# Kernel optimization log

Hardware: AMD Instinct MI355X
Metric: run time of the kernel (lower is better)

Reference implementation:

```python
import jax, jax.numpy as jnp
import numpy as np

B, C, H, W, K = 2, 64, 192, 192, 7
PAD = K // 2
EPS = 1e-6


def _win_idx(L):
    # NATTEN border handling: window is shifted (not zero-padded) to stay in-bounds.
    i = jnp.arange(L)
    start = jnp.clip(i - PAD, 0, L - K)            # [L] window start per query pos
    win = start[:, None] + jnp.arange(K)[None]     # [L,K] absolute key positions
    pb = (K - 1) - (i - start)                     # [L] rpb start index per query pos
    pbi = pb[:, None] + jnp.arange(K)[None]        # [L,K] rpb table indices
    return win, pbi


def setup_inputs() -> dict:
    key = jax.random.key(0)
    ks = jax.random.split(key, 10)
    g = jax.random.normal(ks[0], (B, C, H, W), jnp.float32)
    cd = jax.random.uniform(ks[1], (B, 1, H, W), dtype=jnp.float32)
    dense = jax.random.uniform(ks[2], (B, 1, H, W), dtype=jnp.float32)
    sel = jax.random.uniform(ks[3], (B, 1, H, W)) < 0.05
    sd = jnp.where(sel, dense, 0.0)
    mask = (jax.random.uniform(ks[4], (B, 1, H, W)) < 0.5).astype(jnp.float32)
    ln_w = 1.0 + 0.02 * jax.random.normal(ks[5], (C,), jnp.float32)
    ln_b = 0.02 * jax.random.normal(ks[6], (C,), jnp.float32)
    conv_w = 0.05 * jax.random.normal(ks[7], (2 * C, C + 1), jnp.float32)  # 1x1 conv
    conv_b = 0.02 * jax.random.normal(ks[8], (2 * C,), jnp.float32)
    rpb = 0.02 * jax.random.normal(ks[9], (1, 2 * K - 1, 2 * K - 1), jnp.float32)
    return {"g": g, "cd": cd, "sd": sd, "mask": mask,
            "ln_w": ln_w, "ln_b": ln_b, "conv_w": conv_w, "conv_b": conv_b, "rpb": rpb}


def reference(g, cd, sd, mask, ln_w, ln_b, conv_w, conv_b, rpb):
    # LayerNorm2d: normalize over channel dim per spatial location
    mu = g.mean(axis=1, keepdims=True)
    var = ((g - mu) ** 2).mean(axis=1, keepdims=True)
    gn = (g - mu) * jax.lax.rsqrt(var + EPS)
    gn = gn * ln_w[None, :, None, None] + ln_b[None, :, None, None]

    z = jnp.concatenate([gn, cd], axis=1)                      # [B,C+1,H,W]
    qk = jnp.einsum('bchw,oc->bohw', z, conv_w) + conv_b[None, :, None, None]
    q, k = qk[:, :C], qk[:, C:]
    k = k * mask

    qc = q.transpose(0, 2, 3, 1)                               # [B,H,W,C] single head
    kc = k.transpose(0, 2, 3, 1)
    rwin, rpbi = _win_idx(H)
    cwin, cpbi = _win_idx(W)

    # NATTEN qk + relative position bias over 7x7 neighborhoods
    k_win = kc[:, rwin][:, :, :, cwin]                         # [B,H,K,W,K,C]
    attn = jnp.einsum('bhwc,bhiwjc->bhwij', qc, k_win)         # [B,H,W,K,K]
    bias = rpb[0][rpbi][:, :, cpbi]                            # [H,K,W,K]
    attn = attn + bias.transpose(0, 2, 1, 3)[None]
    a = jax.nn.softmax(attn.reshape(B, H, W, K * K), axis=-1).reshape(B, H, W, K, K)

    # NATTEN av with v = cd (head_dim 1)
    v_win = cd[:, 0][:, rwin][:, :, :, cwin]                   # [B,H,K,W,K]
    cd_out = jnp.einsum('bhwij,bhiwj->bhw', a, v_win)[:, None]  # [B,1,H,W]
    m_win = mask[:, 0][:, rwin][:, :, :, cwin]
    mask_out = jnp.einsum('bhwij,bhiwj->bhw', a, m_win)[:, None]

    # NYU / SDR post-processing
    cd_out = cd_out * mask + cd * (1.0 - mask)
    valid = sd > 0
    cd_out = jnp.where(valid, sd, cd_out)
    mask_out = jnp.where(valid, mask, mask_out)
    return cd_out, mask_out
```

## Files before the change

### kernel.cpp

```cpp
#include <hip/hip_runtime.h>

constexpr int NB = 2;
constexpr int NC = 64;
constexpr int NH = 192;
constexpr int NW = 192;
constexpr int NK = 7;
constexpr int NHW = NH * NW;
constexpr int NPIX = NB * NHW;
constexpr float EPS = 1e-6f;

__global__ __launch_bounds__(256) void qk_gemm(
    const float* __restrict__ g, const float* __restrict__ cd,
    const float* __restrict__ mask,
    const float* __restrict__ ln_w, const float* __restrict__ ln_b,
    const float* __restrict__ conv_w, const float* __restrict__ conv_b,
    float* __restrict__ qbuf, float* __restrict__ kbuf)
{
    __shared__ float Z[65][128];
    __shared__ float WTc[33][128];

    int tid = threadIdx.x;
    int p0 = blockIdx.x * 128;
    int b  = p0 / NHW;
    int hw0 = p0 - b * NHW;

    int px = tid >> 1;
    int hf = tid & 1;
    const float* gp = g + (size_t)(b * NC + hf * 32) * NHW + (hw0 + px);
    float vals[32];
    float s = 0.f, sq = 0.f;
#pragma unroll
    for (int j = 0; j < 32; ++j) {
        float v = gp[(size_t)j * NHW];
        vals[j] = v; s += v; sq += v * v;
    }
    s  += __shfl_xor(s, 1);
    sq += __shfl_xor(sq, 1);
    float mu   = s * (1.f / 64.f);
    float rstd = rsqrtf(sq * (1.f / 64.f) - mu * mu + EPS);
#pragma unroll
    for (int j = 0; j < 32; ++j) {
        int c = hf * 32 + j;
        Z[c][px] = (vals[j] - mu) * rstd * ln_w[c] + ln_b[c];
    }
    if (hf) Z[64][px] = cd[p0 + px];

    int og = tid >> 4;
    int pg = tid & 15;
    float acc[8][8];
#pragma unroll
    for (int oi = 0; oi < 8; ++oi)
#pragma unroll
        for (int pj = 0; pj < 8; ++pj) acc[oi][pj] = 0.f;

    for (int cc = 0; cc < 65; cc += 33) {
        int nr = (65 - cc < 33) ? (65 - cc) : 33;
        __syncthreads();
        if (tid < 128) {
            int o = tid;
            for (int r = 0; r < nr; ++r)
                WTc[r][o] = conv_w[o * 65 + cc + r];
        }
        __syncthreads();
        for (int r = 0; r < nr; ++r) {
            float4 w0 = *(const float4*)&WTc[r][8 * og];
            float4 w1 = *(const float4*)&WTc[r][8 * og + 4];
            float4 z0 = *(const float4*)&Z[cc + r][8 * pg];
            float4 z1 = *(const float4*)&Z[cc + r][8 * pg + 4];
            float w8[8] = {w0.x, w0.y, w0.z, w0.w, w1.x, w1.y, w1.z, w1.w};
            float z8[8] = {z0.x, z0.y, z0.z, z0.w, z1.x, z1.y, z1.z, z1.w};
#pragma unroll
            for (int oi = 0; oi < 8; ++oi)
#pragma unroll
                for (int pj = 0; pj < 8; ++pj)
                    acc[oi][pj] = fmaf(w8[oi], z8[pj], acc[oi][pj]);
        }
    }

    int o0  = og * 8;
    int pxb = pg * 8;
    float4 ba = *(const float4*)&conv_b[o0];
    float4 bb = *(const float4*)&conv_b[o0 + 4];
    float bia[8] = {ba.x, ba.y, ba.z, ba.w, bb.x, bb.y, bb.z, bb.w};
    bool isq = (o0 < 64);
    float m8[8];
    if (!isq) {
        float4 ma = *(const float4*)&mask[p0 + pxb];
        float4 mc = *(const float4*)&mask[p0 + pxb + 4];
        m8[0]=ma.x; m8[1]=ma.y; m8[2]=ma.z; m8[3]=ma.w;
        m8[4]=mc.x; m8[5]=mc.y; m8[6]=mc.z; m8[7]=mc.w;
    }
    float* base = isq ? (qbuf + (size_t)(b * NC + o0) * NHW + hw0 + pxb)
                      : (kbuf + (size_t)(b * NC + o0 - 64) * NHW + hw0 + pxb);
#pragma unroll
    for (int oi = 0; oi < 8; ++oi) {
        float v[8];
#pragma unroll
        for (int pj = 0; pj < 8; ++pj) {
            float t = acc[oi][pj] + bia[oi];
            v[pj] = isq ? t : t * m8[pj];
        }
        float* dst = base + (size_t)oi * NHW;
        *(float4*)&dst[0] = make_float4(v[0], v[1], v[2], v[3]);
        *(float4*)&dst[4] = make_float4(v[4], v[5], v[6], v[7]);
    }
}

__global__ __launch_bounds__(512) void attn_tile(
    const float* __restrict__ qbuf, const float* __restrict__ kbuf,
    const float* __restrict__ cd, const float* __restrict__ sd,
    const float* __restrict__ mask, const float* __restrict__ rpb,
    float* __restrict__ out_cd, float* __restrict__ out_mask)
{
    __shared__ float kst[8][2][240];
    __shared__ float cdt[14 * 24];
    __shared__ float mt [14 * 24];
    __shared__ float rpbt[169];
    __shared__ float xch[128][49];

    int tid  = threadIdx.x;
    int g    = tid >> 6;
    int lane = tid & 63;
    int rq   = g & 1;
    int quar = g >> 1;
    int tx   = lane & 15;
    int tyw  = lane >> 4;

    int bid = blockIdx.x;
    int swz = (bid & 7) * 72 + (bid >> 3);
    int bw = swz % 12;
    int t2 = swz / 12;
    int bh = t2 % 24;
    int b  = t2 / 24;
    int w0 = bw * 16, h0 = bh * 8;
    int hr0 = h0 + rq * 4;

    int h = hr0 + tyw;
    int w = w0 + tx;
    int rs = min(max(h - 3, 0), NH - NK);
    int cs = min(max(w - 3, 0), NW - NK);
    int rb  = (rs - (hr0 - 3)) * 24 + (cs - (w0 - 3));
    int rbB = (rs - (h0  - 3)) * 24 + (cs - (w0 - 3));

    const float* cdb = cd   + (size_t)b * NHW;
    const float* msb = mask + (size_t)b * NHW;
    for (int e = tid; e < 308; e += 512) {
        int r = e / 22, c2 = e - r * 22;
        int gr = min(max(h0 - 3 + r, 0), NH - 1);
        int gc = min(max(w0 - 3 + c2, 0), NW - 1);
        cdt[r * 24 + c2] = cdb[gr * NW + gc];
        mt [r * 24 + c2] = msb[gr * NW + gc];
    }
    if (tid < 169) rpbt[tid] = rpb[tid];

    int soff[4], slds[4]; bool sact[4];
#pragma unroll
    for (int s = 0; s < 4; ++s) {
        int e = lane + 64 * s;
        int r = e / 22, c2 = e - r * 22;
        int gr = min(max(hr0 - 3 + r, 0), NH - 1);
        int gc = min(max(w0 - 3 + c2, 0), NW - 1);
        soff[s] = gr * NW + gc;
        slds[s] = r * 24 + c2;
        sact[s] = (e < 220);
    }

    const float* kb = kbuf + (size_t)(b * NC + quar * 16) * NHW;
    const float* qb = qbuf + (size_t)(b * NC + quar * 16) * NHW + h * NW + w;

    float at[49];
#pragma unroll
    for (int n = 0; n < 49; ++n) at[n] = 0.f;

    float st[4];
#pragma unroll
    for (int s = 0; s < 4; ++s) st[s] = sact[s] ? kb[soff[s]] : 0.f;
    float* k0 = kst[g][0];
    float* k1 = kst[g][1];
#pragma unroll
    for (int s = 0; s < 4; ++s) if (sact[s]) k0[slds[s]] = st[s];
    float qA = qb[0];
    float qB = qb[NHW];

    for (int i = 0; i < 16; ++i) {
        if (i + 1 < 16) {
            const float* kb2 = kb + (size_t)(i + 1) * NHW;
#pragma unroll
            for (int s = 0; s < 4; ++s) st[s] = sact[s] ? kb2[soff[s]] : 0.f;
        }
        float q = qA;
        qA = qB;
        if (i + 2 < 16) qB = qb[(size_t)(i + 2) * NHW];
        const float* kt = ((i & 1) ? k1 : k0) + rb;
#pragma unroll
        for (int r = 0; r < 7; ++r)
#pragma unroll
            for (int j = 0; j < 7; ++j)
                at[r * 7 + j] = fmaf(q, kt[r * 24 + j], at[r * 7 + j]);
        if (i + 1 < 16) {
            float* nk = (i & 1) ? k0 : k1;
#pragma unroll
            for (int s = 0; s < 4; ++s) if (sact[s]) nk[slds[s]] = st[s];
        }
    }

    int pxid = (rq * 4 + tyw) * 16 + tx;
    if (quar == 3) {
#pragma unroll
        for (int n = 0; n < 49; ++n) xch[pxid][n] = at[n];
    }
    __syncthreads();
    if (quar == 2) {
#pragma unroll
        for (int n = 0; n < 49; ++n) xch[pxid][n] += at[n];
    }
    __syncthreads();
    if (quar == 1) {
#pragma unroll
        for (int n = 0; n < 49; ++n) xch[pxid][n] += at[n];
    }
    __syncthreads();
    int pr = 6 - (h - rs);
    int pc = 6 - (w - cs);
    if (quar == 0) {
#pragma unroll
        for (int n = 0; n < 49; ++n) at[n] += xch[pxid][n];
#pragma unroll
        for (int r = 0; r < 7; ++r)
#pragma unroll
            for (int j = 0; j < 7; ++j)
                at[r * 7 + j] += rpbt[(pr + r) * 13 + pc + j];
#pragma unroll
        for (int n = 0; n < 49; ++n) xch[pxid][n] = at[n];
    }
    __syncthreads();
    if (quar >= 2) return;
    if (quar == 1) {
#pragma unroll
        for (int n = 0; n < 49; ++n) at[n] = xch[pxid][n];
    }

    float mx = -1e30f;
#pragma unroll
    for (int n = 0; n < 49; ++n) mx = fmaxf(mx, at[n]);
    float sm = 0.f;
#pragma unroll
    for (int n = 0; n < 49; ++n) {
        at[n] = __expf(at[n] - mx);
        sm += at[n];
    }

    const float* vt = (quar ? mt : cdt) + rbB;
    float sv = 0.f;
#pragma unroll
    for (int r = 0; r < 7; ++r)
#pragma unroll
        for (int j = 0; j < 7; ++j)
            sv = fmaf(at[r * 7 + j], vt[r * 24 + j], sv);
    sv /= sm;

    int p = b * NHW + h * NW + w;
    float sdc = sd[p];
    int cidx = (rq * 4 + tyw + 3) * 24 + (tx + 3);
    float mc = mt[cidx];
    if (quar == 0) {
        float cdc = cdt[cidx];
        float co = sv * mc + cdc * (1.f - mc);
        if (sdc > 0.f) co = sdc;
        out_cd[p] = co;
    } else {
        out_mask[p] = (sdc > 0.f) ? mc : sv;
    }
}

extern "C" void kernel_launch(void* const* d_in, const int* in_sizes, int n_in,
                              void* d_out, int out_size, void* d_ws, size_t ws_size,
                              hipStream_t stream) {
    const float* g      = (const float*)d_in[0];
    const float* cd     = (const float*)d_in[1];
    const float* sd     = (const float*)d_in[2];
    const float* mask   = (const float*)d_in[3];
    const float* ln_w   = (const float*)d_in[4];
    const float* ln_b   = (const float*)d_in[5];
    const float* conv_w = (const float*)d_in[6];
    const float* conv_b = (const float*)d_in[7];
    const float* rpb    = (const float*)d_in[8];

    float* out  = (float*)d_out;
    float* qbuf = (float*)d_ws;
    float* kbuf = qbuf + (size_t)NB * NC * NHW;

    qk_gemm<<<dim3(NPIX / 128), dim3(256), 0, stream>>>(
        g, cd, mask, ln_w, ln_b, conv_w, conv_b, qbuf, kbuf);
    attn_tile<<<dim3(NB * 24 * 12), dim3(512), 0, stream>>>(
        qbuf, kbuf, cd, sd, mask, rpb, out, out + NPIX);
}
```

Before: 147.5 us.

## Compute two adjacent pixels per thread in attention tile to reuse key loads

```diff
diff --git a/kernel.cpp b/kernel.cpp
--- a/kernel.cpp
+++ b/kernel.cpp
@@ -106,25 +106,26 @@
     }
 }
 
-__global__ __launch_bounds__(512) void attn_tile(
+struct TrueC  { static constexpr bool value = true;  };
+struct FalseC { static constexpr bool value = false; };
+
+__global__ __launch_bounds__(256) void attn_tile(
     const float* __restrict__ qbuf, const float* __restrict__ kbuf,
     const float* __restrict__ cd, const float* __restrict__ sd,
     const float* __restrict__ mask, const float* __restrict__ rpb,
     float* __restrict__ out_cd, float* __restrict__ out_mask)
 {
-    __shared__ float kst[8][2][240];
-    __shared__ float cdt[14 * 24];
-    __shared__ float mt [14 * 24];
+    __shared__ float kst[4][2][350];
+    __shared__ float xch[49][2][64];
+    __shared__ float cdt[350];
+    __shared__ float mt [350];
     __shared__ float rpbt[169];
-    __shared__ float xch[128][49];
 
     int tid  = threadIdx.x;
     int g    = tid >> 6;
     int lane = tid & 63;
-    int rq   = g & 1;
-    int quar = g >> 1;
-    int tx   = lane & 15;
-    int tyw  = lane >> 4;
+    int tx   = lane & 7;
+    int ty   = lane >> 3;
 
     int bid = blockIdx.x;
     int swz = (bid & 7) * 72 + (bid >> 3);
@@ -133,143 +134,187 @@
     int bh = t2 % 24;
     int b  = t2 / 24;
     int w0 = bw * 16, h0 = bh * 8;
-    int hr0 = h0 + rq * 4;
-
-    int h = hr0 + tyw;
-    int w = w0 + tx;
-    int rs = min(max(h - 3, 0), NH - NK);
-    int cs = min(max(w - 3, 0), NW - NK);
-    int rb  = (rs - (hr0 - 3)) * 24 + (cs - (w0 - 3));
-    int rbB = (rs - (h0  - 3)) * 24 + (cs - (w0 - 3));
+
+    int h   = h0 + ty;
+    int wpx = w0 + 2 * tx;
+    int rs  = min(max(h - 3, 0), NH - NK);
+    int cs0 = min(max(wpx - 3, 0), NW - NK);
+    int cs1 = min(max(wpx - 2, 0), NW - NK);
+    int d1  = cs1 - cs0;
+    int ktb = (rs - (h0 - 3)) * 25 + (cs0 - (w0 - 3));
 
     const float* cdb = cd   + (size_t)b * NHW;
     const float* msb = mask + (size_t)b * NHW;
-    for (int e = tid; e < 308; e += 512) {
-        int r = e / 22, c2 = e - r * 22;
+    for (int e = tid; e < 308; e += 256) {
+        int r = e / 22, c = e - r * 22;
         int gr = min(max(h0 - 3 + r, 0), NH - 1);
-        int gc = min(max(w0 - 3 + c2, 0), NW - 1);
-        cdt[r * 24 + c2] = cdb[gr * NW + gc];
-        mt [r * 24 + c2] = msb[gr * NW + gc];
+        int gc = min(max(w0 - 3 + c, 0), NW - 1);
+        cdt[r * 25 + c] = cdb[gr * NW + gc];
+        mt [r * 25 + c] = msb[gr * NW + gc];
     }
     if (tid < 169) rpbt[tid] = rpb[tid];
 
-    int soff[4], slds[4]; bool sact[4];
-#pragma unroll
-    for (int s = 0; s < 4; ++s) {
+    int soff[5], slds[5];
+#pragma unroll
+    for (int s = 0; s < 5; ++s) {
         int e = lane + 64 * s;
-        int r = e / 22, c2 = e - r * 22;
-        int gr = min(max(hr0 - 3 + r, 0), NH - 1);
-        int gc = min(max(w0 - 3 + c2, 0), NW - 1);
-        soff[s] = gr * NW + gc;
-        slds[s] = r * 24 + c2;
-        sact[s] = (e < 220);
-    }
-
-    const float* kb = kbuf + (size_t)(b * NC + quar * 16) * NHW;
-    const float* qb = qbuf + (size_t)(b * NC + quar * 16) * NHW + h * NW + w;
-
-    float at[49];
-#pragma unroll
-    for (int n = 0; n < 49; ++n) at[n] = 0.f;
-
-    float st[4];
-#pragma unroll
-    for (int s = 0; s < 4; ++s) st[s] = sact[s] ? kb[soff[s]] : 0.f;
-    float* k0 = kst[g][0];
-    float* k1 = kst[g][1];
-#pragma unroll
-    for (int s = 0; s < 4; ++s) if (sact[s]) k0[slds[s]] = st[s];
-    float qA = qb[0];
-    float qB = qb[NHW];
-
-    for (int i = 0; i < 16; ++i) {
-        if (i + 1 < 16) {
-            const float* kb2 = kb + (size_t)(i + 1) * NHW;
-#pragma unroll
-            for (int s = 0; s < 4; ++s) st[s] = sact[s] ? kb2[soff[s]] : 0.f;
-        }
-        float q = qA;
-        qA = qB;
-        if (i + 2 < 16) qB = qb[(size_t)(i + 2) * NHW];
-        const float* kt = ((i & 1) ? k1 : k0) + rb;
+        int r = e / 22, c = e - r * 22;
+        int gr = min(max(h0 - 3 + r, 0), NH - 1);
+        int gc = min(max(w0 - 3 + c, 0), NW - 1);
+        bool act = e < 308;
+        soff[s] = act ? (gr * NW + gc) : 0;
+        slds[s] = act ? (r * 25 + c) : 348;
+    }
+
+    const float* kb = kbuf + (size_t)(b * NC + g * 16) * NHW;
+    const float* qb = qbuf + (size_t)(b * NC + g * 16) * NHW + h * NW + wpx;
+
+    float at0[49], at1[49];
+#pragma unroll
+    for (int n = 0; n < 49; ++n) { at0[n] = 0.f; at1[n] = 0.f; }
+
+    float* k0 = &kst[g][0][0];
+    float* k1 = &kst[g][1][0];
+
+    auto run = [&](auto edgec) {
+        constexpr bool EDGE = decltype(edgec)::value;
+        float st[5];
+#pragma unroll
+        for (int s = 0; s < 5; ++s) st[s] = kb[soff[s]];
+#pragma unroll
+        for (int s = 0; s < 5; ++s) k0[slds[s]] = st[s];
+        float2 qA = *(const float2*)qb;
+        float2 qB = *(const float2*)(qb + NHW);
+        for (int i = 0; i < 16; ++i) {
+            if (i + 1 < 16) {
+                const float* kb2 = kb + (size_t)(i + 1) * NHW;
+#pragma unroll
+                for (int s = 0; s < 5; ++s) st[s] = kb2[soff[s]];
+            }
+            float2 q = qA; qA = qB;
+            if (i + 2 < 16) qB = *(const float2*)(qb + (size_t)(i + 2) * NHW);
+            const float* kt = ((i & 1) ? k1 : k0) + ktb;
+#pragma unroll
+            for (int r = 0; r < 7; ++r) {
+                const float* kr = kt + r * 25;
+                float v[8];
+#pragma unroll
+                for (int j = 0; j < 8; ++j) v[j] = kr[j];
+#pragma unroll
+                for (int j = 0; j < 7; ++j)
+                    at0[r * 7 + j] = fmaf(q.x, v[j], at0[r * 7 + j]);
+#pragma unroll
+                for (int j = 0; j < 7; ++j) {
+                    float u;
+                    if constexpr (EDGE) u = d1 ? v[j + 1] : v[j];
+                    else                u = v[j + 1];
+                    at1[r * 7 + j] = fmaf(q.y, u, at1[r * 7 + j]);
+                }
+            }
+            if (i + 1 < 16) {
+                float* nk = (i & 1) ? k0 : k1;
+#pragma unroll
+                for (int s = 0; s < 5; ++s) nk[slds[s]] = st[s];
+            }
+        }
+    };
+    if (bw == 0 || bw == 11) run(TrueC{}); else run(FalseC{});
+
+    __syncthreads();
+    if (g == 3) {
+#pragma unroll
+        for (int n = 0; n < 49; ++n) {
+            xch[n][0][lane] = at0[n]; xch[n][1][lane] = at1[n];
+        }
+    }
+    __syncthreads();
+    if (g == 2) {
+#pragma unroll
+        for (int n = 0; n < 49; ++n) {
+            xch[n][0][lane] += at0[n]; xch[n][1][lane] += at1[n];
+        }
+    }
+    __syncthreads();
+    if (g == 0) {
+#pragma unroll
+        for (int n = 0; n < 49; ++n) {
+            xch[n][0][lane] += at0[n]; xch[n][1][lane] += at1[n];
+        }
+    }
+    __syncthreads();
+    int pr  = 6 - (h - rs);
+    int pc0 = 6 - (wpx - cs0);
+    int pc1 = 6 - (wpx + 1 - cs1);
+    if (g == 1) {
+#pragma unroll
+        for (int n = 0; n < 49; ++n) {
+            at0[n] += xch[n][0][lane]; at1[n] += xch[n][1][lane];
+        }
 #pragma unroll
         for (int r = 0; r < 7; ++r)
 #pragma unroll
-            for (int j = 0; j < 7; ++j)
-                at[r * 7 + j] = fmaf(q, kt[r * 24 + j], at[r * 7 + j]);
-        if (i + 1 < 16) {
-            float* nk = (i & 1) ? k0 : k1;
-#pragma unroll
-            for (int s = 0; s < 4; ++s) if (sact[s]) nk[slds[s]] = st[s];
-        }
-    }
-
-    int pxid = (rq * 4 + tyw) * 16 + tx;
-    if (quar == 3) {
-#pragma unroll
-        for (int n = 0; n < 49; ++n) xch[pxid][n] = at[n];
-    }
-    __syncthreads();
-    if (quar == 2) {
-#pragma unroll
-        for (int n = 0; n < 49; ++n) xch[pxid][n] += at[n];
-    }
-    __syncthreads();
-    if (quar == 1) {
-#pragma unroll
-        for (int n = 0; n < 49; ++n) xch[pxid][n] += at[n];
-    }
-    __syncthreads();
-    int pr = 6 - (h - rs);
-    int pc = 6 - (w - cs);
-    if (quar == 0) {
-#pragma unroll
-        for (int n = 0; n < 49; ++n) at[n] += xch[pxid][n];
-#pragma unroll
-        for (int r = 0; r < 7; ++r)
-#pragma unroll
-            for (int j = 0; j < 7; ++j)
-                at[r * 7 + j] += rpbt[(pr + r) * 13 + pc + j];
-#pragma unroll
-        for (int n = 0; n < 49; ++n) xch[pxid][n] = at[n];
-    }
-    __syncthreads();
-    if (quar >= 2) return;
-    if (quar == 1) {
-#pragma unroll
-        for (int n = 0; n < 49; ++n) at[n] = xch[pxid][n];
-    }
-
-    float mx = -1e30f;
-#pragma unroll
-    for (int n = 0; n < 49; ++n) mx = fmaxf(mx, at[n]);
-    float sm = 0.f;
+            for (int j = 0; j < 7; ++j) {
+                at0[r * 7 + j] += rpbt[(pr + r) * 13 + pc0 + j];
+                at1[r * 7 + j] += rpbt[(pr + r) * 13 + pc1 + j];
+            }
+#pragma unroll
+        for (int n = 0; n < 49; ++n) {
+            xch[n][0][lane] = at0[n]; xch[n][1][lane] = at1[n];
+        }
+    }
+    __syncthreads();
+    if (g == 0) {
+#pragma unroll
+        for (int n = 0; n < 49; ++n) {
+            at0[n] = xch[n][0][lane]; at1[n] = xch[n][1][lane];
+        }
+    }
+    if (g >= 2) return;
+
+    float mx0 = -1e30f, mx1 = -1e30f;
 #pragma unroll
     for (int n = 0; n < 49; ++n) {
-        at[n] = __expf(at[n] - mx);
-        sm += at[n];
-    }
-
-    const float* vt = (quar ? mt : cdt) + rbB;
-    float sv = 0.f;
-#pragma unroll
-    for (int r = 0; r < 7; ++r)
-#pragma unroll
-        for (int j = 0; j < 7; ++j)
-            sv = fmaf(at[r * 7 + j], vt[r * 24 + j], sv);
-    sv /= sm;
-
-    int p = b * NHW + h * NW + w;
-    float sdc = sd[p];
-    int cidx = (rq * 4 + tyw + 3) * 24 + (tx + 3);
-    float mc = mt[cidx];
-    if (quar == 0) {
-        float cdc = cdt[cidx];
-        float co = sv * mc + cdc * (1.f - mc);
-        if (sdc > 0.f) co = sdc;
-        out_cd[p] = co;
+        mx0 = fmaxf(mx0, at0[n]); mx1 = fmaxf(mx1, at1[n]);
+    }
+    float sm0 = 0.f, sm1 = 0.f;
+#pragma unroll
+    for (int n = 0; n < 49; ++n) {
+        at0[n] = __expf(at0[n] - mx0); sm0 += at0[n];
+        at1[n] = __expf(at1[n] - mx1); sm1 += at1[n];
+    }
+
+    const float* vt = (g ? mt : cdt) + ktb;
+    float sv0 = 0.f, sv1 = 0.f;
+#pragma unroll
+    for (int r = 0; r < 7; ++r) {
+        const float* vr = vt + r * 25;
+        float v[8];
+#pragma unroll
+        for (int j = 0; j < 8; ++j) v[j] = vr[j];
+#pragma unroll
+        for (int j = 0; j < 7; ++j) {
+            sv0 = fmaf(at0[r * 7 + j], v[j], sv0);
+            float u = d1 ? v[j + 1] : v[j];
+            sv1 = fmaf(at1[r * 7 + j], u, sv1);
+        }
+    }
+    sv0 /= sm0; sv1 /= sm1;
+
+    int p = b * NHW + h * NW + wpx;
+    float2 sdv = *(const float2*)(sd + p);
+    int ci = (ty + 3) * 25 + (2 * tx + 3);
+    float mc0 = mt[ci], mc1 = mt[ci + 1];
+    if (g == 0) {
+        float cdc0 = cdt[ci], cdc1 = cdt[ci + 1];
+        float co0 = sv0 * mc0 + cdc0 * (1.f - mc0);
+        float co1 = sv1 * mc1 + cdc1 * (1.f - mc1);
+        if (sdv.x > 0.f) co0 = sdv.x;
+        if (sdv.y > 0.f) co1 = sdv.y;
+        *(float2*)(out_cd + p) = make_float2(co0, co1);
     } else {
-        out_mask[p] = (sdc > 0.f) ? mc : sv;
+        float o0 = (sdv.x > 0.f) ? mc0 : sv0;
+        float o1 = (sdv.y > 0.f) ? mc1 : sv1;
+        *(float2*)(out_mask + p) = make_float2(o0, o1);
     }
 }
 
@@ -292,6 +337,6 @@
 
     qk_gemm<<<dim3(NPIX / 128), dim3(256), 0, stream>>>(
         g, cd, mask, ln_w, ln_b, conv_w, conv_b, qbuf, kbuf);
-    attn_tile<<<dim3(NB * 24 * 12), dim3(512), 0, stream>>>(
+    attn_tile<<<dim3(NB * 24 * 12), dim3(256), 0, stream>>>(
         qbuf, kbuf, cd, sd, mask, rpb, out, out + NPIX);
 }
```

Result: faster. 135.5 us (median of 2 runs) (-8.1%).
